# Kernel optimization log

Measured on AMD Instinct MI355X. Metric: run time of the kernel, lower is better.

Reference implementation:

```python
import jax, jax.numpy as jnp
import numpy as np
from jax import lax

N_HARM = 64
N_BINS = 64
SR = 16000
B, T = 16, 64000


def setup_inputs() -> dict:
    key = jax.random.key(0)
    ks = jax.random.split(key, 12)
    audio = jax.random.normal(ks[0], (B, T), dtype=jnp.float32)
    # realistic fundamental frequencies in [80, 400) Hz
    f0 = 80.0 + 320.0 * jax.random.uniform(ks[1], (B, T), dtype=jnp.float32)
    white_noise = jax.random.normal(ks[2], (B, T), dtype=jnp.float32)
    def wconv(k, o, i, ksz):
        return jax.random.normal(k, (o, i, ksz), dtype=jnp.float32) * (1.0 / np.sqrt(i * ksz))
    w1 = wconv(ks[3], 32, 1, 9); b1 = jnp.zeros((32,), jnp.float32)
    w2 = wconv(ks[4], 64, 32, 9); b2 = jnp.zeros((64,), jnp.float32)
    w3 = wconv(ks[5], 128, 64, 9); b3 = jnp.zeros((128,), jnp.float32)
    wl = jax.random.normal(ks[6], (N_HARM + N_BINS, 128), dtype=jnp.float32) * (1.0 / np.sqrt(128))
    bl = jnp.zeros((N_HARM + N_BINS,), jnp.float32)
    return {"audio": audio, "f0": f0, "white_noise": white_noise,
            "w1": w1, "b1": b1, "w2": w2, "b2": b2, "w3": w3, "b3": b3,
            "wl": wl, "bl": bl}


def _conv1d(x, w, b):
    # x: [B, C_in, T], w: [C_out, C_in, K]; stride 2, pad 4
    y = lax.conv_general_dilated(x, w, window_strides=(2,), padding=[(4, 4)],
                                 dimension_numbers=("NCH", "OIH", "NCH"))
    return jax.nn.relu(y + b[None, :, None])


def reference(audio, f0, white_noise, w1, b1, w2, b2, w3, b3, wl, bl):
    batch, time = audio.shape
    # --- encoder ---
    x = audio[:, None, :]                    # [B, 1, T]
    x = _conv1d(x, w1, b1)                   # [B, 32, T/2]
    x = _conv1d(x, w2, b2)                   # [B, 64, T/4]
    x = _conv1d(x, w3, b3)                   # [B, 128, T/8]
    pooled = x.mean(axis=2)                  # AdaptiveAvgPool1d(1) + Flatten -> [B, 128]
    feats = pooled @ wl.T + bl               # [B, 128]
    # --- harmonic synth ---
    amps = jax.nn.relu(feats[:, :N_HARM])    # [B, H]; constant over time in original
    amps = amps / (amps.sum(axis=1, keepdims=True) + 1e-6)
    t = jnp.linspace(0.0, time / SR, time)   # endpoint-inclusive, as torch.linspace
    harm_idx = jnp.arange(1, N_HARM + 1, dtype=jnp.float32)
    # phase: [B, H, T] = 2*pi * (h * f0) * t
    phase = (2.0 * jnp.pi) * f0[:, None, :] * harm_idx[None, :, None] * t[None, None, :]
    harmonic_audio = jnp.einsum("bh,bht->bt", amps, jnp.sin(phase))
    # --- noise synth ---
    noise_mag = feats[:, N_HARM:]            # [B, n_bins]; mean over time of a constant = itself
    bin_size = time // N_BINS
    shaped = (white_noise.reshape(batch, N_BINS, bin_size) * noise_mag[:, :, None]).reshape(batch, time)
    return harmonic_audio + shaped
```

## Files before the change

kernel.cpp:

```cpp
#include <hip/hip_runtime.h>
#include <hip/hip_bf16.h>
#include <math.h>

typedef unsigned short u16;
typedef _Float16 f16x8 __attribute__((ext_vector_type(8)));
typedef float    f32x16 __attribute__((ext_vector_type(16)));
typedef u16      u16x8  __attribute__((ext_vector_type(8)));
typedef u16      u16x4  __attribute__((ext_vector_type(4)));

#define BATCH 16
#define T0 64000
#define T1 32000
#define T2 16000
#define T3 8000
#define NT3 250
#define NBLKX 32
#define NROWS1 1040

static __device__ __forceinline__ u16 f2h(float f) {
    _Float16 h = (_Float16)f;
    u16 u;
    __builtin_memcpy(&u, &h, 2);
    return u;
}

__global__ __launch_bounds__(256) void prep_w_k(const float* __restrict__ w2,
                                                const float* __restrict__ w3,
                                                u16* __restrict__ a2t,
                                                u16* __restrict__ a3t,
                                                float* __restrict__ pooled) {
    int idx = blockIdx.x * 256 + threadIdx.x;
    if (idx < 18432) {
        int j = idx & 7, o = (idx >> 3) & 63, g = (idx >> 9) & 3, kk = idx >> 11;
        a2t[idx] = f2h(w2[(o * 32 + g * 8 + j) * 9 + kk]);
    } else if (idx < 18432 + 73728) {
        int jdx = idx - 18432;
        int j = jdx & 7, o = (jdx >> 3) & 127, g = (jdx >> 10) & 7, kk = jdx >> 13;
        a3t[jdx] = f2h(w3[(o * 64 + g * 8 + j) * 9 + kk]);
    } else if (idx < 18432 + 73728 + 2048) {
        pooled[idx - 18432 - 73728] = 0.f;
    }
}

__global__ __launch_bounds__(512, 2) void mega_k(const float* __restrict__ audio,
                                                 const float* __restrict__ w1,
                                                 const float* __restrict__ b1,
                                                 const u16* __restrict__ a2t,
                                                 const float* __restrict__ b2,
                                                 const u16* __restrict__ a3t,
                                                 const float* __restrict__ b3,
                                                 float* __restrict__ pooled) {
    __shared__ u16 sm[520 * 64];
    const int tid = threadIdx.x;
    const int b = blockIdx.y;
    const int r0 = blockIdx.x * NT3;
    const int lane = tid & 63, wv = tid >> 6;
    const int ls = lane >> 5, ln = lane & 31;

    {
        const float* ar = audio + (size_t)b * T0;
        #pragma unroll
        for (int rep = 0; rep < 3; ++rep) {
            int l1 = rep * 512 + tid;
            if (l1 >= NROWS1) break;
            int t1 = 4 * r0 - 12 + l1;
            int rr = l1 >> 1, pp = l1 & 1;
            if (t1 < 0 || t1 >= T1) {
                u16x8 z;
                #pragma unroll
                for (int q = 0; q < 8; ++q) z[q] = 0;
                #pragma unroll
                for (int g = 0; g < 4; ++g) {
                    int slot = (pp * 4 + g) ^ (rr & 7);
                    *(u16x8*)(sm + rr * 64 + slot * 8) = z;
                }
            } else {
                int base = 2 * t1 - 4;
                float x[9];
                #pragma unroll
                for (int k = 0; k < 9; ++k) {
                    int t0v = base + k;
                    x[k] = (t0v >= 0 && t0v < T0) ? ar[t0v] : 0.f;
                }
                #pragma unroll
                for (int g = 0; g < 4; ++g) {
                    u16x8 v;
                    #pragma unroll
                    for (int j = 0; j < 8; ++j) {
                        int ch = g * 8 + j;
                        float acc = b1[ch];
                        #pragma unroll
                        for (int k = 0; k < 9; ++k) acc = fmaf(x[k], w1[ch * 9 + k], acc);
                        v[j] = f2h(fmaxf(acc, 0.f));
                    }
                    int slot = (pp * 4 + g) ^ (rr & 7);
                    *(u16x8*)(sm + rr * 64 + slot * 8) = v;
                }
            }
        }
    }
    __syncthreads();

    for (int cc = 0; cc < 2; ++cc) {
        int nl = cc * 256 + 32 * wv + ln;
        f32x16 acc2[2];
        #pragma unroll
        for (int mi = 0; mi < 2; ++mi)
            #pragma unroll
            for (int q = 0; q < 16; ++q) acc2[mi][q] = 0.f;
        f16x8 bfB[2];
        #pragma unroll 3
        for (int kk = 0; kk < 9; ++kk) {
            {
                int rr = nl + (kk >> 1);
                int pp = kk & 1;
                #pragma unroll
                for (int step = 0; step < 2; ++step) {
                    int slot = (pp * 4 + 2 * step + ls) ^ (rr & 7);
                    bfB[step] = *(const f16x8*)(sm + rr * 64 + slot * 8);
                }
            }
            const u16* ap = a2t + kk * 2048;
            #pragma unroll
            for (int step = 0; step < 2; ++step) {
                f16x8 af0 = *(const f16x8*)(ap + (2 * step + ls) * 512 + ln * 8);
                f16x8 af1 = *(const f16x8*)(ap + (2 * step + ls) * 512 + (32 + ln) * 8);
                acc2[0] = __builtin_amdgcn_mfma_f32_32x32x16_f16(af0, bfB[step], acc2[0], 0, 0, 0);
                acc2[1] = __builtin_amdgcn_mfma_f32_32x32x16_f16(af1, bfB[step], acc2[1], 0, 0, 0);
            }
        }
        __syncthreads();
        int l2 = nl;
        int t2 = 2 * r0 - 4 + l2;
        bool valid = (t2 >= 0) && (t2 < T2);
        #pragma unroll
        for (int mi = 0; mi < 2; ++mi)
            #pragma unroll
            for (int q = 0; q < 4; ++q) {
                u16x4 v;
                #pragma unroll
                for (int d = 0; d < 4; ++d) {
                    int o = 32 * mi + 8 * q + 4 * ls + d;
                    float xv = valid ? fmaxf(acc2[mi][4 * q + d] + b2[o], 0.f) : 0.f;
                    v[d] = f2h(xv);
                }
                int gy = 4 * mi + q;
                int sy = gy ^ ((l2 >> 1) & 7);
                *(u16x4*)(sm + l2 * 64 + sy * 8 + ls * 4) = v;
            }
        __syncthreads();
    }

    const int mh = wv & 1, nh = wv >> 1;
    f32x16 acc3[2][2];
    #pragma unroll
    for (int mi = 0; mi < 2; ++mi)
        #pragma unroll
        for (int ni = 0; ni < 2; ++ni)
            #pragma unroll
            for (int q = 0; q < 16; ++q) acc3[mi][ni][q] = 0.f;

    f16x8 bf[2][4];
    #pragma unroll 3
    for (int kk = 0; kk < 9; ++kk) {
        const u16* ap = a3t + kk * 8192;
        {
            #pragma unroll
            for (int ni = 0; ni < 2; ++ni) {
                int nl = 64 * nh + 32 * ni + ln;
                int l2 = 2 * nl + kk;
                int rrC = nl + (kk >> 1);
                #pragma unroll
                for (int step = 0; step < 4; ++step) {
                    int sy = (2 * step + ls) ^ (rrC & 7);
                    bf[ni][step] = *(const f16x8*)(sm + l2 * 64 + sy * 8);
                }
            }
        }
        #pragma unroll
        for (int step = 0; step < 4; ++step) {
            f16x8 af0 = *(const f16x8*)(ap + (2 * step + ls) * 1024 + (64 * mh + ln) * 8);
            f16x8 af1 = *(const f16x8*)(ap + (2 * step + ls) * 1024 + (64 * mh + 32 + ln) * 8);
            #pragma unroll
            for (int ni = 0; ni < 2; ++ni) {
                acc3[0][ni] = __builtin_amdgcn_mfma_f32_32x32x16_f16(af0, bf[ni][step], acc3[0][ni], 0, 0, 0);
                acc3[1][ni] = __builtin_amdgcn_mfma_f32_32x32x16_f16(af1, bf[ni][step], acc3[1][ni], 0, 0, 0);
            }
        }
    }

    float loc[32];
    #pragma unroll
    for (int mi = 0; mi < 2; ++mi)
        #pragma unroll
        for (int r = 0; r < 16; ++r) {
            int o = 64 * mh + 32 * mi + (r & 3) + 8 * (r >> 2) + 4 * ls;
            float bias = b3[o];
            float s = 0.f;
            #pragma unroll
            for (int ni = 0; ni < 2; ++ni) {
                int nl = 64 * nh + 32 * ni + ln;
                float v = fmaxf(acc3[mi][ni][r] + bias, 0.f);
                s += (nl < NT3) ? v : 0.f;
            }
            loc[mi * 16 + r] = s;
        }
    __syncthreads();
    float* smf = (float*)sm;
    #pragma unroll
    for (int mi = 0; mi < 2; ++mi)
        #pragma unroll
        for (int r = 0; r < 16; ++r) {
            int o = 64 * mh + 32 * mi + (r & 3) + 8 * (r >> 2) + 4 * ls;
            smf[nh * 4096 + o * 32 + ln] = loc[mi * 16 + r];
        }
    __syncthreads();
    if (tid < 128) {
        int o = tid;
        float s = 0.f;
        #pragma unroll
        for (int j = 0; j < 32; ++j) {
            int col = (j + o) & 31;
            s += smf[o * 32 + col] + smf[4096 + o * 32 + col]
               + smf[8192 + o * 32 + col] + smf[12288 + o * 32 + col];
        }
        atomicAdd(&pooled[b * 128 + o], s);
    }
}

__global__ __launch_bounds__(256) void synth_k(const float* __restrict__ f0,
                                               const float* __restrict__ wn,
                                               const float* __restrict__ pooled,
                                               const float* __restrict__ wl,
                                               const float* __restrict__ bl,
                                               float* __restrict__ out) {
    int tid = threadIdx.x;
    int b = blockIdx.y;
    __shared__ float pl[128];
    __shared__ float red[64];
    __shared__ float sa[64];
    __shared__ float nm[64];
    if (tid < 128) pl[tid] = pooled[b * 128 + tid] * (1.0f / 8000.0f);
    __syncthreads();
    float feat = 0.f;
    if (tid < 128) {
        feat = bl[tid];
        #pragma unroll 8
        for (int i = 0; i < 128; ++i) feat = fmaf(pl[i], wl[tid * 128 + i], feat);
    }
    if (tid < 64) red[tid] = fmaxf(feat, 0.f);
    __syncthreads();
    if (tid < 32) red[tid] += red[tid + 32];
    __syncthreads();
    if (tid < 16) red[tid] += red[tid + 16];
    __syncthreads();
    if (tid < 8) red[tid] += red[tid + 8];
    __syncthreads();
    if (tid < 4) red[tid] += red[tid + 4];
    __syncthreads();
    if (tid < 2) red[tid] += red[tid + 2];
    __syncthreads();
    if (tid == 0) red[0] += red[1];
    __syncthreads();
    float denom = red[0] + 1e-6f;
    if (tid < 64) sa[tid] = fmaxf(feat, 0.f) / denom;
    else if (tid < 128) nm[tid - 64] = feat;
    __syncthreads();
    int t = blockIdx.x * 256 + tid;
    float f0v = f0[(size_t)b * T0 + t];
    double u = (double)f0v * ((double)t * (4.0 / 63999.0));
    float uf = (float)(u - floor(u));
    float acc = 0.f;
    #pragma unroll
    for (int h = 1; h <= 64; ++h) {
        float x = uf * (float)h;
        x = x - floorf(x);
        acc = fmaf(sa[h - 1], __builtin_amdgcn_sinf(x), acc);
    }
    out[(size_t)b * T0 + t] = acc + wn[(size_t)b * T0 + t] * nm[t / 1000];
}

extern "C" void kernel_launch(void* const* d_in, const int* in_sizes, int n_in,
                              void* d_out, int out_size, void* d_ws, size_t ws_size,
                              hipStream_t stream) {
    const float* audio = (const float*)d_in[0];
    const float* f0    = (const float*)d_in[1];
    const float* wn    = (const float*)d_in[2];
    const float* w1    = (const float*)d_in[3];
    const float* b1    = (const float*)d_in[4];
    const float* w2    = (const float*)d_in[5];
    const float* b2    = (const float*)d_in[6];
    const float* w3    = (const float*)d_in[7];
    const float* b3    = (const float*)d_in[8];
    const float* wl    = (const float*)d_in[9];
    const float* bl    = (const float*)d_in[10];
    float* out = (float*)d_out;

    char* ws = (char*)d_ws;
    float* pooled = (float*)(ws);
    u16* a2t = (u16*)(ws + 8192);
    u16* a3t = (u16*)(ws + 8192 + 36864);

    prep_w_k<<<368, 256, 0, stream>>>(w2, w3, a2t, a3t, pooled);
    mega_k<<<dim3(NBLKX, BATCH), 512, 0, stream>>>(audio, w1, b1, a2t, b2, a3t, b3, pooled);
    synth_k<<<dim3(T0 / 256, BATCH), 256, 0, stream>>>(f0, wn, pooled, wl, bl, out);
}
```

Measured before the change: 155.2 us.

## Compute head linear layer once in last encoder block; merge conv2 chunks

Moves the pooled-to-features linear layer, ReLU and amplitude normalisation out of every synth block. They now run once in the last-finishing encoder block, found with an atomic counter and threadfence. Synth blocks then load only the precomputed amps and noise magnitudes. The conv2 stage also processes both 256-column chunks in one k-loop with doubled accumulators, sharing A-fragment loads and cutting a sync pair. This adds a serial tail in one block and more register pressure in conv2.

```diff
diff --git a/kernel.cpp b/kernel.cpp
--- a/kernel.cpp
+++ b/kernel.cpp
@@ -16,6 +16,7 @@
 #define NT3 250
 #define NBLKX 32
 #define NROWS1 1040
+#define NMEGA (NBLKX * BATCH)
 
 static __device__ __forceinline__ u16 f2h(float f) {
     _Float16 h = (_Float16)f;
@@ -28,7 +29,8 @@
                                                 const float* __restrict__ w3,
                                                 u16* __restrict__ a2t,
                                                 u16* __restrict__ a3t,
-                                                float* __restrict__ pooled) {
+                                                float* __restrict__ pooled,
+                                                int* __restrict__ counter) {
     int idx = blockIdx.x * 256 + threadIdx.x;
     if (idx < 18432) {
         int j = idx & 7, o = (idx >> 3) & 63, g = (idx >> 9) & 3, kk = idx >> 11;
@@ -39,6 +41,8 @@
         a3t[jdx] = f2h(w3[(o * 64 + g * 8 + j) * 9 + kk]);
     } else if (idx < 18432 + 73728 + 2048) {
         pooled[idx - 18432 - 73728] = 0.f;
+    } else if (idx == 18432 + 73728 + 2048) {
+        *counter = 0;
     }
 }
 
@@ -49,8 +53,14 @@
                                                  const float* __restrict__ b2,
                                                  const u16* __restrict__ a3t,
                                                  const float* __restrict__ b3,
-                                                 float* __restrict__ pooled) {
+                                                 float* __restrict__ pooled,
+                                                 int* __restrict__ counter,
+                                                 const float* __restrict__ wl,
+                                                 const float* __restrict__ bl,
+                                                 float* __restrict__ amps,
+                                                 float* __restrict__ nmag) {
     __shared__ u16 sm[520 * 64];
+    __shared__ int s_last;
     const int tid = threadIdx.x;
     const int b = blockIdx.y;
     const int r0 = blockIdx.x * NT3;
@@ -101,23 +111,25 @@
     }
     __syncthreads();
 
-    for (int cc = 0; cc < 2; ++cc) {
-        int nl = cc * 256 + 32 * wv + ln;
-        f32x16 acc2[2];
-        #pragma unroll
-        for (int mi = 0; mi < 2; ++mi)
-            #pragma unroll
-            for (int q = 0; q < 16; ++q) acc2[mi][q] = 0.f;
-        f16x8 bfB[2];
+    {
+        f32x16 acc2[2][2];
+        #pragma unroll
+        for (int ch = 0; ch < 2; ++ch)
+            #pragma unroll
+            for (int mi = 0; mi < 2; ++mi)
+                #pragma unroll
+                for (int q = 0; q < 16; ++q) acc2[ch][mi][q] = 0.f;
+        f16x8 bfB[2][2];
         #pragma unroll 3
         for (int kk = 0; kk < 9; ++kk) {
-            {
-                int rr = nl + (kk >> 1);
-                int pp = kk & 1;
+            int kh = kk >> 1, pp = kk & 1;
+            #pragma unroll
+            for (int ch = 0; ch < 2; ++ch) {
+                int line = ch * 256 + 32 * wv + ln + kh;
                 #pragma unroll
                 for (int step = 0; step < 2; ++step) {
-                    int slot = (pp * 4 + 2 * step + ls) ^ (rr & 7);
-                    bfB[step] = *(const f16x8*)(sm + rr * 64 + slot * 8);
+                    int slot = (pp * 4 + 2 * step + ls) ^ (line & 7);
+                    bfB[ch][step] = *(const f16x8*)(sm + line * 64 + slot * 8);
                 }
             }
             const u16* ap = a2t + kk * 2048;
@@ -125,29 +137,35 @@
             for (int step = 0; step < 2; ++step) {
                 f16x8 af0 = *(const f16x8*)(ap + (2 * step + ls) * 512 + ln * 8);
                 f16x8 af1 = *(const f16x8*)(ap + (2 * step + ls) * 512 + (32 + ln) * 8);
-                acc2[0] = __builtin_amdgcn_mfma_f32_32x32x16_f16(af0, bfB[step], acc2[0], 0, 0, 0);
-                acc2[1] = __builtin_amdgcn_mfma_f32_32x32x16_f16(af1, bfB[step], acc2[1], 0, 0, 0);
-            }
-        }
-        __syncthreads();
-        int l2 = nl;
-        int t2 = 2 * r0 - 4 + l2;
-        bool valid = (t2 >= 0) && (t2 < T2);
-        #pragma unroll
-        for (int mi = 0; mi < 2; ++mi)
-            #pragma unroll
-            for (int q = 0; q < 4; ++q) {
-                u16x4 v;
-                #pragma unroll
-                for (int d = 0; d < 4; ++d) {
-                    int o = 32 * mi + 8 * q + 4 * ls + d;
-                    float xv = valid ? fmaxf(acc2[mi][4 * q + d] + b2[o], 0.f) : 0.f;
-                    v[d] = f2h(xv);
-                }
-                int gy = 4 * mi + q;
-                int sy = gy ^ ((l2 >> 1) & 7);
-                *(u16x4*)(sm + l2 * 64 + sy * 8 + ls * 4) = v;
-            }
+                #pragma unroll
+                for (int ch = 0; ch < 2; ++ch) {
+                    acc2[ch][0] = __builtin_amdgcn_mfma_f32_32x32x16_f16(af0, bfB[ch][step], acc2[ch][0], 0, 0, 0);
+                    acc2[ch][1] = __builtin_amdgcn_mfma_f32_32x32x16_f16(af1, bfB[ch][step], acc2[ch][1], 0, 0, 0);
+                }
+            }
+        }
+        __syncthreads();
+        #pragma unroll
+        for (int ch = 0; ch < 2; ++ch) {
+            int l2 = ch * 256 + 32 * wv + ln;
+            int t2 = 2 * r0 - 4 + l2;
+            bool valid = (t2 >= 0) && (t2 < T2);
+            #pragma unroll
+            for (int mi = 0; mi < 2; ++mi)
+                #pragma unroll
+                for (int q = 0; q < 4; ++q) {
+                    u16x4 v;
+                    #pragma unroll
+                    for (int d = 0; d < 4; ++d) {
+                        int o = 32 * mi + 8 * q + 4 * ls + d;
+                        float xv = valid ? fmaxf(acc2[ch][mi][4 * q + d] + b2[o], 0.f) : 0.f;
+                        v[d] = f2h(xv);
+                    }
+                    int gy = 4 * mi + q;
+                    int sy = gy ^ ((l2 >> 1) & 7);
+                    *(u16x4*)(sm + l2 * 64 + sy * 8 + ls * 4) = v;
+                }
+        }
         __syncthreads();
     }
 
@@ -164,17 +182,15 @@
     #pragma unroll 3
     for (int kk = 0; kk < 9; ++kk) {
         const u16* ap = a3t + kk * 8192;
-        {
-            #pragma unroll
-            for (int ni = 0; ni < 2; ++ni) {
-                int nl = 64 * nh + 32 * ni + ln;
-                int l2 = 2 * nl + kk;
-                int rrC = nl + (kk >> 1);
-                #pragma unroll
-                for (int step = 0; step < 4; ++step) {
-                    int sy = (2 * step + ls) ^ (rrC & 7);
-                    bf[ni][step] = *(const f16x8*)(sm + l2 * 64 + sy * 8);
-                }
+        #pragma unroll
+        for (int ni = 0; ni < 2; ++ni) {
+            int nl = 64 * nh + 32 * ni + ln;
+            int l2 = 2 * nl + kk;
+            int rrC = nl + (kk >> 1);
+            #pragma unroll
+            for (int step = 0; step < 4; ++step) {
+                int sy = (2 * step + ls) ^ (rrC & 7);
+                bf[ni][step] = *(const f16x8*)(sm + l2 * 64 + sy * 8);
             }
         }
         #pragma unroll
@@ -226,45 +242,63 @@
         }
         atomicAdd(&pooled[b * 128 + o], s);
     }
+
+    if (tid == 0) {
+        __threadfence();
+        int old = atomicAdd(counter, 1);
+        s_last = (old == NMEGA - 1) ? 1 : 0;
+    }
+    __syncthreads();
+    if (s_last) {
+        __threadfence();
+        for (int i = tid; i < 2048; i += 512) smf[i] = pooled[i] * (1.0f / 8000.0f);
+        __syncthreads();
+        float ft[4];
+        #pragma unroll
+        for (int r = 0; r < 4; ++r) {
+            int id = tid + r * 512;
+            int bb = id >> 7, oo = id & 127;
+            float acc = bl[oo];
+            #pragma unroll 8
+            for (int i = 0; i < 128; ++i) acc = fmaf(smf[bb * 128 + i], wl[oo * 128 + i], acc);
+            ft[r] = acc;
+        }
+        __syncthreads();
+        #pragma unroll
+        for (int r = 0; r < 4; ++r) {
+            int id = tid + r * 512;
+            int bb = id >> 7, oo = id & 127;
+            if (oo < 64) smf[2048 + bb * 64 + oo] = fmaxf(ft[r], 0.f);
+            else         nmag[bb * 64 + (oo - 64)] = ft[r];
+        }
+        __syncthreads();
+        if (tid < 16) {
+            float s = 0.f;
+            #pragma unroll 8
+            for (int j = 0; j < 64; ++j) s += smf[2048 + tid * 64 + j];
+            smf[3072 + tid] = s + 1e-6f;
+        }
+        __syncthreads();
+        #pragma unroll
+        for (int r = 0; r < 4; ++r) {
+            int id = tid + r * 512;
+            int bb = id >> 7, oo = id & 127;
+            if (oo < 64) amps[bb * 64 + oo] = fmaxf(ft[r], 0.f) / smf[3072 + bb];
+        }
+    }
 }
 
 __global__ __launch_bounds__(256) void synth_k(const float* __restrict__ f0,
                                                const float* __restrict__ wn,
-                                               const float* __restrict__ pooled,
-                                               const float* __restrict__ wl,
-                                               const float* __restrict__ bl,
+                                               const float* __restrict__ amps,
+                                               const float* __restrict__ nmag,
                                                float* __restrict__ out) {
     int tid = threadIdx.x;
     int b = blockIdx.y;
-    __shared__ float pl[128];
-    __shared__ float red[64];
     __shared__ float sa[64];
-    __shared__ float nm[64];
-    if (tid < 128) pl[tid] = pooled[b * 128 + tid] * (1.0f / 8000.0f);
-    __syncthreads();
-    float feat = 0.f;
-    if (tid < 128) {
-        feat = bl[tid];
-        #pragma unroll 8
-        for (int i = 0; i < 128; ++i) feat = fmaf(pl[i], wl[tid * 128 + i], feat);
-    }
-    if (tid < 64) red[tid] = fmaxf(feat, 0.f);
-    __syncthreads();
-    if (tid < 32) red[tid] += red[tid + 32];
-    __syncthreads();
-    if (tid < 16) red[tid] += red[tid + 16];
-    __syncthreads();
-    if (tid < 8) red[tid] += red[tid + 8];
-    __syncthreads();
-    if (tid < 4) red[tid] += red[tid + 4];
-    __syncthreads();
-    if (tid < 2) red[tid] += red[tid + 2];
-    __syncthreads();
-    if (tid == 0) red[0] += red[1];
-    __syncthreads();
-    float denom = red[0] + 1e-6f;
-    if (tid < 64) sa[tid] = fmaxf(feat, 0.f) / denom;
-    else if (tid < 128) nm[tid - 64] = feat;
+    __shared__ float nm2[64];
+    if (tid < 64) sa[tid] = amps[b * 64 + tid];
+    else if (tid < 128) nm2[tid - 64] = nmag[b * 64 + (tid - 64)];
     __syncthreads();
     int t = blockIdx.x * 256 + tid;
     float f0v = f0[(size_t)b * T0 + t];
@@ -277,7 +311,7 @@
         x = x - floorf(x);
         acc = fmaf(sa[h - 1], __builtin_amdgcn_sinf(x), acc);
     }
-    out[(size_t)b * T0 + t] = acc + wn[(size_t)b * T0 + t] * nm[t / 1000];
+    out[(size_t)b * T0 + t] = acc + wn[(size_t)b * T0 + t] * nm2[t / 1000];
 }
 
 extern "C" void kernel_launch(void* const* d_in, const int* in_sizes, int n_in,
@@ -297,11 +331,15 @@
     float* out = (float*)d_out;
 
     char* ws = (char*)d_ws;
-    float* pooled = (float*)(ws);
-    u16* a2t = (u16*)(ws + 8192);
-    u16* a3t = (u16*)(ws + 8192 + 36864);
-
-    prep_w_k<<<368, 256, 0, stream>>>(w2, w3, a2t, a3t, pooled);
-    mega_k<<<dim3(NBLKX, BATCH), 512, 0, stream>>>(audio, w1, b1, a2t, b2, a3t, b3, pooled);
-    synth_k<<<dim3(T0 / 256, BATCH), 256, 0, stream>>>(f0, wn, pooled, wl, bl, out);
-}
+    float* pooled  = (float*)(ws);
+    float* amps    = (float*)(ws + 8192);
+    float* nmag    = (float*)(ws + 12288);
+    int*   counter = (int*)(ws + 16384);
+    u16* a2t = (u16*)(ws + 16448);
+    u16* a3t = (u16*)(ws + 16448 + 36864);
+
+    prep_w_k<<<369, 256, 0, stream>>>(w2, w3, a2t, a3t, pooled, counter);
+    mega_k<<<dim3(NBLKX, BATCH), 512, 0, stream>>>(audio, w1, b1, a2t, b2, a3t, b3,
+                                                   pooled, counter, wl, bl, amps, nmag);
+    synth_k<<<dim3(T0 / 256, BATCH), 256, 0, stream>>>(f0, wn, amps, nmag, out);
+}
```

Measured after the change: 165.1 us. 6.4% more time.
